# Kernel tuning notes

Hardware: AMD Instinct MI355X
Metric: run time of the kernel (lower is better)

Reference implementation:

```python
import jax, jax.numpy as jnp
import numpy as np
from math import factorial, sqrt

L_MAX = 3
MUL = 64
# e3nn FullyConnectedTensorProduct instruction order: lexicographic over (l1, l2, l3)
# keeping paths with triangle inequality and matching parity ((-1)^(l1+l2) == (-1)^l3).
PATHS = [(l1, l2, l3)
         for l1 in range(L_MAX + 1)
         for l2 in range(L_MAX + 1)
         for l3 in range(L_MAX + 1)
         if abs(l1 - l2) <= l3 <= l1 + l2 and (l1 + l2 + l3) % 2 == 0]
assert len(PATHS) == 23
N_TO = {l3: sum(1 for p in PATHS if p[2] == l3) for l3 in range(L_MAX + 1)}


def _su2_cg(j1, m1, j2, m2, j3, m3):
    # Complex-basis Clebsch-Gordan coefficient (Racah formula), as in e3nn.
    if m3 != m1 + m2:
        return 0.0
    f = factorial
    vmin = max(-j1 + j2 + m3, -j1 + m1, 0)
    vmax = min(j2 + j3 + m1, j3 - j1 + j2, j3 + m3)
    c = sqrt((2 * j3 + 1) * f(j3 + j1 - j2) * f(j3 - j1 + j2) * f(j1 + j2 - j3)
             * f(j3 + m3) * f(j3 - m3)
             / (f(j1 + j2 + j3 + 1) * f(j1 - m1) * f(j1 + m1) * f(j2 - m2) * f(j2 + m2)))
    s = 0.0
    for v in range(vmin, vmax + 1):
        s += (-1) ** (v + j2 + m2) / f(v) * f(j2 + j3 + m1 - v) * f(j1 - m1 + v) \
             / f(j3 - j1 + j2 - v) / f(j3 + m3 - v) / f(v + j1 - j2 - m3)
    return c * s


def _q(l):
    # Change of basis real -> complex spherical harmonics (e3nn convention).
    q = np.zeros((2 * l + 1, 2 * l + 1), dtype=np.complex128)
    for m in range(-l, 0):
        q[l + m, l + abs(m)] = 1.0 / np.sqrt(2.0)
        q[l + m, l - abs(m)] = -1j / np.sqrt(2.0)
    q[l, l] = 1.0
    for m in range(1, l + 1):
        q[l + m, l + abs(m)] = (-1) ** m / np.sqrt(2.0)
        q[l + m, l - abs(m)] = 1j * (-1) ** m / np.sqrt(2.0)
    return (-1j) ** l * q


def _w3j(l1, l2, l3):
    # Real-basis Wigner 3j tensor, unit Frobenius norm (e3nn's o3.wigner_3j).
    csu2 = np.zeros((2 * l1 + 1, 2 * l2 + 1, 2 * l3 + 1))
    for m1 in range(-l1, l1 + 1):
        for m2 in range(-l2, l2 + 1):
            m3 = m1 + m2
            if -l3 <= m3 <= l3:
                csu2[l1 + m1, l2 + m2, l3 + m3] = _su2_cg(l1, m1, l2, m2, l3, m3)
    q1, q2, q3 = _q(l1), _q(l2), _q(l3)
    c = np.einsum('ij,kl,mn,ikn->jlm', q1, q2, np.conj(q3.T), csu2.astype(np.complex128))
    c = np.real(c)
    return (c / np.linalg.norm(c)).astype(np.float32)


W3J = {p: jnp.asarray(_w3j(*p)) for p in PATHS}
# e3nn 'component' irrep_normalization + 'element' path_normalization:
# per-path coeff = sqrt(ir_out.dim / (n_paths_into_out * mul1 * mul2)).
COEFF = {p: float(np.sqrt((2 * p[2] + 1) / (N_TO[p[2]] * MUL * MUL))) for p in PATHS}


def setup_inputs():
    key = jax.random.key(0)
    kx, kw = jax.random.split(key)
    x = jax.random.normal(kx, (2, 1024, MUL * (L_MAX + 1) ** 2), dtype=jnp.float32)
    weights = jax.random.normal(kw, (len(PATHS), MUL, MUL, MUL), dtype=jnp.float32)
    return {"x": x, "weights": weights}


def reference(x, weights):
    B, N, D = x.shape
    Z = B * N
    xf = x.reshape(Z, D)
    # e3nn layout: blocks of (mul, 2l+1) concatenated over l; offset = MUL * l^2.
    xs = [xf[:, MUL * l * l: MUL * (l + 1) ** 2].reshape(Z, MUL, 2 * l + 1)
          for l in range(L_MAX + 1)]
    acc = [jnp.zeros((Z, MUL, 2 * l + 1), dtype=x.dtype) for l in range(L_MAX + 1)]
    for p, (l1, l2, l3) in enumerate(PATHS):
        c = W3J[(l1, l2, l3)]
        t1 = jnp.einsum('zui,ijk->zujk', xs[l1], c)            # [Z,u,2l2+1,2l3+1]
        t2 = jnp.einsum('zujk,zvj->zuvk', t1, xs[l2])          # [Z,u,v,2l3+1]
        seg = jnp.einsum('zuvk,uvw->zwk', t2, weights[p]) * COEFF[(l1, l2, l3)]
        acc[l3] = acc[l3] + seg
    out = jnp.concatenate([a.reshape(Z, -1) for a in acc], axis=-1)
    return out.reshape(B, N, -1)
```

## Files before the change

### kernel.cpp

```cpp
#include <hip/hip_runtime.h>

struct CD { double re, im; };
constexpr CD cmul(CD a, CD b){ return CD{a.re*b.re - a.im*b.im, a.re*b.im + a.im*b.re}; }
constexpr CD conj_(CD a){ return CD{a.re, -a.im}; }

constexpr double factd(int n){ double r = 1.0; for(int i = 2; i <= n; ++i) r *= (double)i; return r; }
constexpr double csqrt_(double x){
  if (x <= 0.0) return 0.0;
  double g = x > 1.0 ? x : 1.0;
  for (int i = 0; i < 100; ++i) g = 0.5*(g + x/g);
  return g;
}

constexpr double su2_cg(int j1,int m1,int j2,int m2,int j3,int m3){
  if (m3 != m1 + m2) return 0.0;
  int vmin = -j1 + j2 + m3;
  if (-j1 + m1 > vmin) vmin = -j1 + m1;
  if (0 > vmin) vmin = 0;
  int vmax = j2 + j3 + m1;
  if (j3 - j1 + j2 < vmax) vmax = j3 - j1 + j2;
  if (j3 + m3 < vmax) vmax = j3 + m3;
  double c = csqrt_((2.0*j3 + 1.0) * factd(j3 + j1 - j2) * factd(j3 - j1 + j2) * factd(j1 + j2 - j3)
                    * factd(j3 + m3) * factd(j3 - m3)
                    / (factd(j1 + j2 + j3 + 1) * factd(j1 - m1) * factd(j1 + m1)
                       * factd(j2 - m2) * factd(j2 + m2)));
  double s = 0.0;
  for (int v = vmin; v <= vmax; ++v){
    double t = (((v + j2 + m2) & 1) ? -1.0 : 1.0) / factd(v)
               * factd(j2 + j3 + m1 - v) * factd(j1 - m1 + v)
               / factd(j3 - j1 + j2 - v) / factd(j3 + m3 - v) / factd(v + j1 - j2 - m3);
    s += t;
  }
  return c * s;
}

struct QM { CD m[7][7]; };
constexpr QM qmat(int l){
  QM q{};
  double is2 = 1.0 / csqrt_(2.0);
  for (int mm = -l; mm < 0; ++mm){
    q.m[l+mm][l-mm] = CD{is2, 0.0};
    q.m[l+mm][l+mm] = CD{0.0, -is2};
  }
  q.m[l][l] = CD{1.0, 0.0};
  for (int mm = 1; mm <= l; ++mm){
    double sgn = (mm & 1) ? -1.0 : 1.0;
    q.m[l+mm][l+mm] = CD{sgn*is2, 0.0};
    q.m[l+mm][l-mm] = CD{0.0, sgn*is2};
  }
  CD ph = (l % 4 == 0) ? CD{1,0} : (l % 4 == 1) ? CD{0,-1} : (l % 4 == 2) ? CD{-1,0} : CD{0,1};
  for (int r = 0; r < 7; ++r)
    for (int c = 0; c < 7; ++c)
      q.m[r][c] = cmul(ph, q.m[r][c]);
  return q;
}

template<int L1,int L2,int L3> struct W3JT { float v[2*L1+1][2*L2+1][2*L3+1]; };

template<int L1,int L2,int L3>
constexpr W3JT<L1,L2,L3> make_w3j(){
  constexpr int D1 = 2*L1+1, D2 = 2*L2+1, D3 = 2*L3+1;
  QM q1 = qmat(L1), q2 = qmat(L2), q3 = qmat(L3);
  double cg[7][7] = {};
  for (int i = 0; i < D1; ++i)
    for (int k = 0; k < D2; ++k){
      int n = i + k - L1 - L2 + L3;
      if (n >= 0 && n < D3) cg[i][k] = su2_cg(L1, i-L1, L2, k-L2, L3, (i-L1)+(k-L2));
    }
  double c[D1][D2][D3] = {};
  double norm2 = 0.0;
  for (int j = 0; j < D1; ++j)
    for (int l = 0; l < D2; ++l)
      for (int m = 0; m < D3; ++m){
        CD s{0.0, 0.0};
        for (int i = 0; i < D1; ++i)
          for (int k = 0; k < D2; ++k){
            double g = cg[i][k];
            if (g == 0.0) continue;
            int n = i + k - L1 - L2 + L3;
            CD t = cmul(q1.m[i][j], q2.m[k][l]);
            t = cmul(t, conj_(q3.m[n][m]));
            s.re += t.re * g; s.im += t.im * g;
          }
        c[j][l][m] = s.re;
        norm2 += s.re * s.re;
      }
  double inv = 1.0 / csqrt_(norm2);
  W3JT<L1,L2,L3> w{};
  for (int j = 0; j < D1; ++j)
    for (int l = 0; l < D2; ++l)
      for (int m = 0; m < D3; ++m){
        double val = c[j][l][m] * inv;
        if (val < 1e-10 && val > -1e-10) val = 0.0;
        w.v[j][l][m] = (float)val;
      }
  return w;
}

__device__ __constant__ int L3P_[23]  = {0,1,2,3,1,0,2,1,3,2,2,1,3,0,2,1,3,3,2,1,3,0,2};
__device__ __constant__ int SWAPP_[23] = {0,1,1,1,0,0,0,1,1,1,0,0,0,0,0,1,1,0,0,0,0,0,0};
constexpr int K3CUM[24] = {0,1,4,9,16,19,20,25,28,35,40,45,48,55,56,61,64,71,78,83,86,93,94,99};
constexpr size_t KSLICE = 2048ull * 64ull;

typedef __bf16 bf16x8 __attribute__((ext_vector_type(8)));
typedef float  f32x4  __attribute__((ext_vector_type(4)));
typedef float  f32x2  __attribute__((ext_vector_type(2)));

__global__ void pack_w_kernel(const float* __restrict__ w, unsigned short* __restrict__ wp, int total){
  int idx = blockIdx.x * 256 + threadIdx.x;
  if (idx >= total) return;
  int e    = idx & 7;
  int lane = (idx >> 3) & 63;
  int nt   = (idx >> 9) & 3;
  int hf   = (idx >> 11) & 1;
  int s    = (idx >> 12) & 63;
  int p    = idx >> 18;
  int kv = hf*32 + (lane >> 4)*8 + e;
  int wc = nt*16 + (lane & 15);
  int l3 = L3P_[p];
  const float nto[4] = {4.f, 6.f, 7.f, 6.f};
  float coeff = sqrtf((2.f*l3 + 1.f) / (nto[l3] * 4096.f));
  int a = SWAPP_[p] ? kv : s;
  int b = SWAPP_[p] ? s : kv;
  float val = w[(((size_t)p*64 + a)*64 + b)*64 + wc] * coeff;
  unsigned bits = __builtin_bit_cast(unsigned, val);
  unsigned r = (bits + 0x7FFFu + ((bits >> 16) & 1u)) >> 16;
  wp[idx] = (unsigned short)r;
}

__global__ void transpose_x(const float* __restrict__ x, float* __restrict__ xT){
  __shared__ float t[32][33];
  int bx = blockIdx.x, by = blockIdx.y;
  int tx = threadIdx.x & 31, ty = threadIdx.x >> 5;
  #pragma unroll
  for (int r = 0; r < 4; ++r)
    t[ty + r*8][tx] = x[(size_t)(by*32 + ty + r*8)*1024 + bx*32 + tx];
  __syncthreads();
  #pragma unroll
  for (int r = 0; r < 4; ++r)
    xT[(size_t)(bx*32 + ty + r*8)*2048 + by*32 + tx] = t[tx][ty + r*8];
}

template<int P,int L1,int L2,int L3,bool SWAP,int G0,int G,bool PART>
__device__ __forceinline__ void run_slot(
    int tile, const float* __restrict__ xT,
    const unsigned short* __restrict__ wp,
    float* __restrict__ dst, float* red)
{
  constexpr int K3 = 2*L3+1;
  constexpr int LK = SWAP ? L1 : L2;
  constexpr int LS = SWAP ? L2 : L1;
  constexpr int DK = 2*LK+1, DS = 2*LS+1;
  constexpr auto C = make_w3j<L1,L2,L3>();

  const int lane = threadIdx.x & 63;
  const int wv   = threadIdx.x >> 6;
  const int zc   = tile*16 + (lane & 15);

  f32x2 xk2[4][DK];
  {
    const float* xkb = xT + (size_t)(64*LK*LK)*2048 + zc;
    const int t0 = wv*32 + (lane >> 4)*8;
    #pragma unroll
    for (int q = 0; q < 4; ++q)
      #pragma unroll
      for (int t = 0; t < DK; ++t){
        float lo = xkb[(size_t)((t0 + 2*q    )*DK + t)*2048];
        float hi = xkb[(size_t)((t0 + 2*q + 1)*DK + t)*2048];
        xk2[q][t] = f32x2{lo, hi};
      }
  }

  const float* xsb = xT + (size_t)(64*LS*LS)*2048 + zc;
  const unsigned short* wu = wp + (size_t)P*262144 + (size_t)wv*2048 + (size_t)lane*8;

  f32x4 acc[G][4];
  #pragma unroll
  for (int a = 0; a < G; ++a)
    #pragma unroll
    for (int b = 0; b < 4; ++b) acc[a][b] = f32x4{0.f,0.f,0.f,0.f};

  auto compute = [&](const bf16x8 (&bf)[4], const float (&xs)[DS]){
    #pragma unroll
    for (int kk = 0; kk < G; ++kk){
      float dk[DK];
      #pragma unroll
      for (int t = 0; t < DK; ++t) dk[t] = 0.f;
      #pragma unroll
      for (int t = 0; t < DK; ++t){
        #pragma unroll
        for (int j = 0; j < DS; ++j){
          const float cv = SWAP ? C.v[t][j][G0+kk] : C.v[j][t][G0+kk];
          if (cv != 0.0f) dk[t] = __builtin_fmaf(xs[j], cv, dk[t]);
        }
      }
      f32x2 af2[4];
      #pragma unroll
      for (int q = 0; q < 4; ++q) af2[q] = f32x2{0.f, 0.f};
      #pragma unroll
      for (int t = 0; t < DK; ++t){
        const f32x2 d2 = f32x2{dk[t], dk[t]};
        #pragma unroll
        for (int q = 0; q < 4; ++q)
          af2[q] += xk2[q][t] * d2;
      }
      bf16x8 af;
      #pragma unroll
      for (int q = 0; q < 4; ++q){
        af[2*q]   = (__bf16)af2[q].x;
        af[2*q+1] = (__bf16)af2[q].y;
      }
      __builtin_amdgcn_s_setprio(1);
      #pragma unroll
      for (int nt = 0; nt < 4; ++nt)
        acc[kk][nt] = __builtin_amdgcn_mfma_f32_16x16x32_bf16(af, bf[nt], acc[kk][nt], 0, 0, 0);
      __builtin_amdgcn_s_setprio(0);
    }
  };

  bf16x8 bA[4], bB[4];
  float xsA[DS], xsB[DS];
  #pragma unroll
  for (int nt = 0; nt < 4; ++nt)
    bA[nt] = *reinterpret_cast<const bf16x8*>(wu + nt*512);
  #pragma unroll
  for (int j = 0; j < DS; ++j) xsA[j] = xsb[(size_t)j*2048];

  for (int s = 0; s < 64; s += 2){
    #pragma unroll
    for (int nt = 0; nt < 4; ++nt)
      bB[nt] = *reinterpret_cast<const bf16x8*>(wu + 4096 + nt*512);
    #pragma unroll
    for (int j = 0; j < DS; ++j) xsB[j] = xsb[(size_t)(DS + j)*2048];

    compute(bA, xsA);

    #pragma unroll
    for (int nt = 0; nt < 4; ++nt)
      bA[nt] = *reinterpret_cast<const bf16x8*>(wu + 8192 + nt*512);
    #pragma unroll
    for (int j = 0; j < DS; ++j) xsA[j] = xsb[(size_t)(2*DS + j)*2048];

    compute(bB, xsB);

    wu  += 8192;
    xsb += (size_t)2*DS*2048;
  }

  constexpr int Gh = (G + 1) / 2;
  static_assert(Gh <= 3, "red[] sized for Gh<=3");
  auto store_one = [&](int kk, int nt, const f32x4& o, const f32x4& a){
    #pragma unroll
    for (int r = 0; r < 4; ++r){
      int zl = ((lane >> 4) << 2) + r;
      int wc = nt*16 + (lane & 15);
      float val = a[r] + o[r];
      if constexpr (PART){
        dst[(size_t)(K3CUM[P] + G0 + kk)*KSLICE + (size_t)(tile*16 + zl)*64 + wc] = val;
      } else {
        unsafeAtomicAdd(dst + (size_t)(tile*16 + zl)*1024 + 64*L3*L3 + wc*K3 + (G0+kk), val);
      }
    }
  };

  if (wv == 1){
    #pragma unroll
    for (int kk = 0; kk < Gh; ++kk)
      #pragma unroll
      for (int nt = 0; nt < 4; ++nt)
        *reinterpret_cast<f32x4*>(&red[((kk*4 + nt)*64 + lane)*4]) = acc[kk][nt];
  }
  __syncthreads();
  if (wv == 0){
    #pragma unroll
    for (int kk = 0; kk < Gh; ++kk)
      #pragma unroll
      for (int nt = 0; nt < 4; ++nt){
        f32x4 o = *reinterpret_cast<const f32x4*>(&red[((kk*4 + nt)*64 + lane)*4]);
        store_one(kk, nt, o, acc[kk][nt]);
      }
  }
  if constexpr (G > Gh){
    if (wv == 0){
      #pragma unroll
      for (int kk = Gh; kk < G; ++kk)
        #pragma unroll
        for (int nt = 0; nt < 4; ++nt)
          *reinterpret_cast<f32x4*>(&red[(((kk-Gh)*4 + nt)*64 + lane)*4]) = acc[kk][nt];
    }
    __syncthreads();
    if (wv == 1){
      #pragma unroll
      for (int kk = Gh; kk < G; ++kk)
        #pragma unroll
        for (int nt = 0; nt < 4; ++nt){
          f32x4 o = *reinterpret_cast<const f32x4*>(&red[(((kk-Gh)*4 + nt)*64 + lane)*4]);
          store_one(kk, nt, o, acc[kk][nt]);
        }
    }
  }
}

template<bool PART>
__global__ __launch_bounds__(128, 3) void tp_main(const float* __restrict__ xT,
    const unsigned short* __restrict__ wp, float* __restrict__ dst)
{
  __shared__ __align__(16) float red[3072];
  const int slot = blockIdx.x >> 7;
  const int tile = blockIdx.x & 127;
  switch (slot){
    case 0:  run_slot< 6,1,1,2,false,0,5,PART>(tile,xT,wp,dst,red); break;
    case 1:  run_slot<16,2,3,3,true ,0,3,PART>(tile,xT,wp,dst,red); break;
    case 2:  run_slot<20,3,2,3,false,0,3,PART>(tile,xT,wp,dst,red); break;
    case 3:  run_slot<14,2,2,2,false,0,3,PART>(tile,xT,wp,dst,red); break;
    case 4:  run_slot<15,2,3,1,true ,0,3,PART>(tile,xT,wp,dst,red); break;
    case 5:  run_slot<19,3,2,1,false,0,3,PART>(tile,xT,wp,dst,red); break;
    case 6:  run_slot< 8,1,2,3,true ,0,4,PART>(tile,xT,wp,dst,red); break;
    case 7:  run_slot<12,2,1,3,false,0,4,PART>(tile,xT,wp,dst,red); break;
    case 8:  run_slot<22,3,3,2,false,0,2,PART>(tile,xT,wp,dst,red); break;
    case 9:  run_slot<22,3,3,2,false,2,2,PART>(tile,xT,wp,dst,red); break;
    case 10: run_slot< 9,1,3,2,true ,0,3,PART>(tile,xT,wp,dst,red); break;
    case 11: run_slot<16,2,3,3,true ,3,2,PART>(tile,xT,wp,dst,red); break;
    case 12: run_slot<16,2,3,3,true ,5,2,PART>(tile,xT,wp,dst,red); break;
    case 13: run_slot<20,3,2,3,false,3,2,PART>(tile,xT,wp,dst,red); break;
    case 14: run_slot<20,3,2,3,false,5,2,PART>(tile,xT,wp,dst,red); break;
    case 15: run_slot< 2,0,2,2,true ,0,5,PART>(tile,xT,wp,dst,red); break;
    case 16: run_slot<10,2,0,2,false,0,5,PART>(tile,xT,wp,dst,red); break;
    case 17: run_slot<11,2,1,1,false,0,3,PART>(tile,xT,wp,dst,red); break;
    case 18: run_slot< 7,1,2,1,true ,0,3,PART>(tile,xT,wp,dst,red); break;
    case 19: run_slot<18,3,1,2,false,0,3,PART>(tile,xT,wp,dst,red); break;
    case 20: run_slot< 8,1,2,3,true ,4,3,PART>(tile,xT,wp,dst,red); break;
    case 21: run_slot<12,2,1,3,false,4,3,PART>(tile,xT,wp,dst,red); break;
    case 22: run_slot<14,2,2,2,false,3,2,PART>(tile,xT,wp,dst,red); break;
    case 23: run_slot< 9,1,3,2,true ,3,2,PART>(tile,xT,wp,dst,red); break;
    case 24: run_slot<18,3,1,2,false,3,2,PART>(tile,xT,wp,dst,red); break;
    case 25: run_slot<22,3,3,2,false,4,1,PART>(tile,xT,wp,dst,red); break;
    case 26: run_slot<21,3,3,0,false,0,1,PART>(tile,xT,wp,dst,red); break;
    case 27: run_slot< 3,0,3,3,true ,0,4,PART>(tile,xT,wp,dst,red); break;
    case 28: run_slot<17,3,0,3,false,0,4,PART>(tile,xT,wp,dst,red); break;
    case 29: run_slot< 3,0,3,3,true ,4,3,PART>(tile,xT,wp,dst,red); break;
    case 30: run_slot<17,3,0,3,false,4,3,PART>(tile,xT,wp,dst,red); break;
    case 31: run_slot< 1,0,1,1,true ,0,3,PART>(tile,xT,wp,dst,red); break;
    case 32: run_slot< 4,1,0,1,false,0,3,PART>(tile,xT,wp,dst,red); break;
    case 33: run_slot<13,2,2,0,false,0,1,PART>(tile,xT,wp,dst,red); break;
    case 34: run_slot< 5,1,1,0,false,0,1,PART>(tile,xT,wp,dst,red); break;
    case 35: run_slot< 0,0,0,0,false,0,1,PART>(tile,xT,wp,dst,red); break;
    default: break;
  }
}

__global__ void gather_out(const float* __restrict__ part, float* __restrict__ out){
  const int z = blockIdx.x;
  const int t = threadIdx.x;
  const int w = t & 63;
  const int g = t >> 6;
  const size_t zw = (size_t)z*64 + w;
  const float* pb = part;
  auto rd = [&](int kg){ return pb[(size_t)kg*KSLICE + zw]; };
  float* ob = out + (size_t)z*1024;
  if (g == 0){
    ob[w] = rd(K3CUM[0]) + rd(K3CUM[5]) + rd(K3CUM[13]) + rd(K3CUM[21]);
  } else if (g == 1){
    #pragma unroll
    for (int k = 0; k < 3; ++k)
      ob[64 + w*3 + k] = rd(K3CUM[1]+k) + rd(K3CUM[4]+k) + rd(K3CUM[7]+k)
                       + rd(K3CUM[11]+k) + rd(K3CUM[15]+k) + rd(K3CUM[19]+k);
  } else if (g == 2){
    #pragma unroll
    for (int k = 0; k < 5; ++k)
      ob[256 + w*5 + k] = rd(K3CUM[2]+k) + rd(K3CUM[6]+k) + rd(K3CUM[9]+k)
                        + rd(K3CUM[10]+k) + rd(K3CUM[14]+k) + rd(K3CUM[18]+k)
                        + rd(K3CUM[22]+k);
  } else {
    #pragma unroll
    for (int k = 0; k < 7; ++k)
      ob[576 + w*7 + k] = rd(K3CUM[3]+k) + rd(K3CUM[8]+k) + rd(K3CUM[12]+k)
                        + rd(K3CUM[16]+k) + rd(K3CUM[17]+k) + rd(K3CUM[20]+k);
  }
}

extern "C" void kernel_launch(void* const* d_in, const int* in_sizes, int n_in,
                              void* d_out, int out_size, void* d_ws, size_t ws_size,
                              hipStream_t stream)
{
  const float* x = (const float*)d_in[0];
  const float* w = (const float*)d_in[1];
  float* out = (float*)d_out;

  const size_t packB = 23ull*64*2*4*64*8 * sizeof(unsigned short);
  const size_t xTB   = 1024ull*2048*sizeof(float);
  const size_t partB = 99ull*KSLICE*sizeof(float);
  const size_t slack = 65536;
  const int totalW = 23*64*2*4*64*8;

  unsigned short* wp = (unsigned short*)d_ws;
  float* xT   = (float*)((char*)d_ws + packB);
  float* part = (float*)((char*)d_ws + packB + xTB);

  if (ws_size < packB + xTB + slack) return;

  pack_w_kernel<<<(totalW + 255)/256, 256, 0, stream>>>(w, wp, totalW);
  dim3 tg(32, 64);
  transpose_x<<<tg, 256, 0, stream>>>(x, xT);

  if (ws_size >= packB + xTB + partB + slack){
    tp_main<true><<<36*128, 128, 0, stream>>>(xT, wp, part);
    gather_out<<<2048, 256, 0, stream>>>(part, out);
  } else {
    hipMemsetAsync(d_out, 0, (size_t)out_size * sizeof(float), stream);
    tp_main<false><<<36*128, 128, 0, stream>>>(xT, wp, out);
  }
}
```

Baseline: 222.7 us.

## Split work so each wave owns a full K range for two z-tiles

Most blocks now use a run_full path in which each of the two waves handles its own 16-row z tile and covers both K halves of the weight, which removes the cross-wave LDS reduction and one barrier. The m3 components are regrouped into many more slots, mostly G=1 or 2. Only the 3-3-x paths keep the half-K split with a sequential reduction. The partial buffer layout changes to (z, k, w) ordering, staged through LDS for coalesced stores, and the double-buffered prefetch loop is replaced by a single-step prefetch. In exchange, weight fragments are reloaded more times in total and register pressure rises from holding both K-half x fragments.

After: 228.5 us. 2.6% more time.

```diff
diff --git a/kernel.cpp b/kernel.cpp
--- a/kernel.cpp
+++ b/kernel.cpp
@@ -100,7 +100,7 @@
 __device__ __constant__ int L3P_[23]  = {0,1,2,3,1,0,2,1,3,2,2,1,3,0,2,1,3,3,2,1,3,0,2};
 __device__ __constant__ int SWAPP_[23] = {0,1,1,1,0,0,0,1,1,1,0,0,0,0,0,1,1,0,0,0,0,0,0};
 constexpr int K3CUM[24] = {0,1,4,9,16,19,20,25,28,35,40,45,48,55,56,61,64,71,78,83,86,93,94,99};
-constexpr size_t KSLICE = 2048ull * 64ull;
+constexpr size_t PSLICE = 2048ull * 64ull;
 
 typedef __bf16 bf16x8 __attribute__((ext_vector_type(8)));
 typedef float  f32x4  __attribute__((ext_vector_type(4)));
@@ -142,7 +142,139 @@
 }
 
 template<int P,int L1,int L2,int L3,bool SWAP,int G0,int G,bool PART>
-__device__ __forceinline__ void run_slot(
+__device__ __forceinline__ void run_full(
+    int tile2, const float* __restrict__ xT,
+    const unsigned short* __restrict__ wp,
+    float* __restrict__ dst, float* lds)
+{
+  constexpr int K3 = 2*L3+1;
+  constexpr int LK = SWAP ? L1 : L2;
+  constexpr int LS = SWAP ? L2 : L1;
+  constexpr int DK = 2*LK+1, DS = 2*LS+1;
+  constexpr auto C = make_w3j<L1,L2,L3>();
+
+  const int lane = threadIdx.x & 63;
+  const int wid  = threadIdx.x >> 6;
+  const int z0   = (tile2*2 + wid)*16;
+  const int zc   = z0 + (lane & 15);
+
+  f32x2 xkl[4][DK], xkh[4][DK];
+  {
+    const float* xkb = xT + (size_t)(64*LK*LK)*2048 + zc;
+    const int t0 = (lane >> 4)*8;
+    #pragma unroll
+    for (int q = 0; q < 4; ++q)
+      #pragma unroll
+      for (int t = 0; t < DK; ++t){
+        xkl[q][t] = f32x2{ xkb[(size_t)((t0 + 2*q    )*DK + t)*2048],
+                           xkb[(size_t)((t0 + 2*q + 1)*DK + t)*2048] };
+        xkh[q][t] = f32x2{ xkb[(size_t)((32 + t0 + 2*q    )*DK + t)*2048],
+                           xkb[(size_t)((32 + t0 + 2*q + 1)*DK + t)*2048] };
+      }
+  }
+
+  const float* xsp = xT + (size_t)(64*LS*LS)*2048 + zc;
+  const unsigned short* wu = wp + (size_t)P*262144 + (size_t)lane*8;
+
+  f32x4 acc[G][4];
+  #pragma unroll
+  for (int a = 0; a < G; ++a)
+    #pragma unroll
+    for (int b = 0; b < 4; ++b) acc[a][b] = f32x4{0.f,0.f,0.f,0.f};
+
+  float xs[DS];
+  #pragma unroll
+  for (int j = 0; j < DS; ++j) xs[j] = xsp[(size_t)j*2048];
+
+  for (int s = 0; s < 64; ++s){
+    bf16x8 bl[4], bh[4];
+    #pragma unroll
+    for (int nt = 0; nt < 4; ++nt){
+      bl[nt] = *reinterpret_cast<const bf16x8*>(wu + nt*512);
+      bh[nt] = *reinterpret_cast<const bf16x8*>(wu + 2048 + nt*512);
+    }
+    const float* xnp = (s < 63) ? xsp + (size_t)DS*2048 : xsp;
+    float xn[DS];
+    #pragma unroll
+    for (int j = 0; j < DS; ++j) xn[j] = xnp[(size_t)j*2048];
+
+    #pragma unroll
+    for (int kk = 0; kk < G; ++kk){
+      float dk[DK];
+      #pragma unroll
+      for (int t = 0; t < DK; ++t) dk[t] = 0.f;
+      #pragma unroll
+      for (int t = 0; t < DK; ++t){
+        #pragma unroll
+        for (int j = 0; j < DS; ++j){
+          const float cv = SWAP ? C.v[t][j][G0+kk] : C.v[j][t][G0+kk];
+          if (cv != 0.0f) dk[t] = __builtin_fmaf(xs[j], cv, dk[t]);
+        }
+      }
+      f32x2 al2[4], ah2[4];
+      #pragma unroll
+      for (int q = 0; q < 4; ++q){ al2[q] = f32x2{0.f,0.f}; ah2[q] = f32x2{0.f,0.f}; }
+      #pragma unroll
+      for (int t = 0; t < DK; ++t){
+        const f32x2 d2 = f32x2{dk[t], dk[t]};
+        #pragma unroll
+        for (int q = 0; q < 4; ++q){
+          al2[q] += xkl[q][t] * d2;
+          ah2[q] += xkh[q][t] * d2;
+        }
+      }
+      bf16x8 afl, afh;
+      #pragma unroll
+      for (int q = 0; q < 4; ++q){
+        afl[2*q] = (__bf16)al2[q].x;  afl[2*q+1] = (__bf16)al2[q].y;
+        afh[2*q] = (__bf16)ah2[q].x;  afh[2*q+1] = (__bf16)ah2[q].y;
+      }
+      __builtin_amdgcn_s_setprio(1);
+      #pragma unroll
+      for (int nt = 0; nt < 4; ++nt){
+        acc[kk][nt] = __builtin_amdgcn_mfma_f32_16x16x32_bf16(afl, bl[nt], acc[kk][nt], 0, 0, 0);
+        acc[kk][nt] = __builtin_amdgcn_mfma_f32_16x16x32_bf16(afh, bh[nt], acc[kk][nt], 0, 0, 0);
+      }
+      __builtin_amdgcn_s_setprio(0);
+    }
+    #pragma unroll
+    for (int j = 0; j < DS; ++j) xs[j] = xn[j];
+    xsp += (size_t)DS*2048;
+    wu  += 4096;
+  }
+
+  if constexpr (PART){
+    float* tl = lds + wid*1040;
+    #pragma unroll
+    for (int kk = 0; kk < G; ++kk){
+      #pragma unroll
+      for (int nt = 0; nt < 4; ++nt)
+        #pragma unroll
+        for (int r = 0; r < 4; ++r)
+          tl[((lane>>4)*4 + r)*65 + nt*16 + (lane & 15)] = acc[kk][nt][r];
+      #pragma unroll
+      for (int zr = 0; zr < 16; ++zr){
+        float v = tl[zr*65 + lane];
+        dst[(size_t)K3CUM[P]*PSLICE + ((size_t)(z0 + zr)*K3 + (G0+kk))*64 + lane] = v;
+      }
+    }
+  } else {
+    #pragma unroll
+    for (int kk = 0; kk < G; ++kk)
+      #pragma unroll
+      for (int nt = 0; nt < 4; ++nt)
+        #pragma unroll
+        for (int r = 0; r < 4; ++r){
+          int zl = (lane>>4)*4 + r;
+          int wc = nt*16 + (lane & 15);
+          unsafeAtomicAdd(dst + (size_t)(z0 + zl)*1024 + 64*L3*L3 + wc*K3 + (G0+kk),
+                          acc[kk][nt][r]);
+        }
+  }
+}
+
+template<int P,int L1,int L2,int L3,bool SWAP,int G0,int G,bool PART>
+__device__ __forceinline__ void run_half(
     int tile, const float* __restrict__ xT,
     const unsigned short* __restrict__ wp,
     float* __restrict__ dst, float* red)
@@ -152,6 +284,7 @@
   constexpr int LS = SWAP ? L2 : L1;
   constexpr int DK = 2*LK+1, DS = 2*LS+1;
   constexpr auto C = make_w3j<L1,L2,L3>();
+  static_assert(G <= 2, "run_half sized for G<=2");
 
   const int lane = threadIdx.x & 63;
   const int wv   = threadIdx.x >> 6;
@@ -164,14 +297,12 @@
     #pragma unroll
     for (int q = 0; q < 4; ++q)
       #pragma unroll
-      for (int t = 0; t < DK; ++t){
-        float lo = xkb[(size_t)((t0 + 2*q    )*DK + t)*2048];
-        float hi = xkb[(size_t)((t0 + 2*q + 1)*DK + t)*2048];
-        xk2[q][t] = f32x2{lo, hi};
-      }
-  }
-
-  const float* xsb = xT + (size_t)(64*LS*LS)*2048 + zc;
+      for (int t = 0; t < DK; ++t)
+        xk2[q][t] = f32x2{ xkb[(size_t)((t0 + 2*q    )*DK + t)*2048],
+                           xkb[(size_t)((t0 + 2*q + 1)*DK + t)*2048] };
+  }
+
+  const float* xsp = xT + (size_t)(64*LS*LS)*2048 + zc;
   const unsigned short* wu = wp + (size_t)P*262144 + (size_t)wv*2048 + (size_t)lane*8;
 
   f32x4 acc[G][4];
@@ -180,7 +311,21 @@
     #pragma unroll
     for (int b = 0; b < 4; ++b) acc[a][b] = f32x4{0.f,0.f,0.f,0.f};
 
-  auto compute = [&](const bf16x8 (&bf)[4], const float (&xs)[DS]){
+  float xs[DS];
+  #pragma unroll
+  for (int j = 0; j < DS; ++j) xs[j] = xsp[(size_t)j*2048];
+
+  for (int s = 0; s < 64; ++s){
+    bf16x8 bfrag[4];
+    #pragma unroll
+    for (int nt = 0; nt < 4; ++nt)
+      bfrag[nt] = *reinterpret_cast<const bf16x8*>(wu + nt*512);
+
+    const float* xnp = (s < 63) ? xsp + (size_t)DS*2048 : xsp;
+    float xn[DS];
+    #pragma unroll
+    for (int j = 0; j < DS; ++j) xn[j] = xnp[(size_t)j*2048];
+
     #pragma unroll
     for (int kk = 0; kk < G; ++kk){
       float dk[DK];
@@ -213,42 +358,15 @@
       __builtin_amdgcn_s_setprio(1);
       #pragma unroll
       for (int nt = 0; nt < 4; ++nt)
-        acc[kk][nt] = __builtin_amdgcn_mfma_f32_16x16x32_bf16(af, bf[nt], acc[kk][nt], 0, 0, 0);
+        acc[kk][nt] = __builtin_amdgcn_mfma_f32_16x16x32_bf16(af, bfrag[nt], acc[kk][nt], 0, 0, 0);
       __builtin_amdgcn_s_setprio(0);
     }
-  };
-
-  bf16x8 bA[4], bB[4];
-  float xsA[DS], xsB[DS];
-  #pragma unroll
-  for (int nt = 0; nt < 4; ++nt)
-    bA[nt] = *reinterpret_cast<const bf16x8*>(wu + nt*512);
-  #pragma unroll
-  for (int j = 0; j < DS; ++j) xsA[j] = xsb[(size_t)j*2048];
-
-  for (int s = 0; s < 64; s += 2){
-    #pragma unroll
-    for (int nt = 0; nt < 4; ++nt)
-      bB[nt] = *reinterpret_cast<const bf16x8*>(wu + 4096 + nt*512);
-    #pragma unroll
-    for (int j = 0; j < DS; ++j) xsB[j] = xsb[(size_t)(DS + j)*2048];
-
-    compute(bA, xsA);
-
-    #pragma unroll
-    for (int nt = 0; nt < 4; ++nt)
-      bA[nt] = *reinterpret_cast<const bf16x8*>(wu + 8192 + nt*512);
-    #pragma unroll
-    for (int j = 0; j < DS; ++j) xsA[j] = xsb[(size_t)(2*DS + j)*2048];
-
-    compute(bB, xsB);
-
-    wu  += 8192;
-    xsb += (size_t)2*DS*2048;
-  }
-
-  constexpr int Gh = (G + 1) / 2;
-  static_assert(Gh <= 3, "red[] sized for Gh<=3");
+    #pragma unroll
+    for (int j = 0; j < DS; ++j) xs[j] = xn[j];
+    xsp += (size_t)DS*2048;
+    wu  += 4096;
+  }
+
   auto store_one = [&](int kk, int nt, const f32x4& o, const f32x4& a){
     #pragma unroll
     for (int r = 0; r < 4; ++r){
@@ -256,7 +374,7 @@
       int wc = nt*16 + (lane & 15);
       float val = a[r] + o[r];
       if constexpr (PART){
-        dst[(size_t)(K3CUM[P] + G0 + kk)*KSLICE + (size_t)(tile*16 + zl)*64 + wc] = val;
+        dst[(size_t)K3CUM[P]*PSLICE + ((size_t)(tile*16 + zl)*K3 + (G0+kk))*64 + wc] = val;
       } else {
         unsafeAtomicAdd(dst + (size_t)(tile*16 + zl)*1024 + 64*L3*L3 + wc*K3 + (G0+kk), val);
       }
@@ -265,38 +383,31 @@
 
   if (wv == 1){
     #pragma unroll
-    for (int kk = 0; kk < Gh; ++kk)
-      #pragma unroll
-      for (int nt = 0; nt < 4; ++nt)
-        *reinterpret_cast<f32x4*>(&red[((kk*4 + nt)*64 + lane)*4]) = acc[kk][nt];
+    for (int nt = 0; nt < 4; ++nt)
+      *reinterpret_cast<f32x4*>(&red[(nt*64 + lane)*4]) = acc[0][nt];
   }
   __syncthreads();
   if (wv == 0){
     #pragma unroll
-    for (int kk = 0; kk < Gh; ++kk)
-      #pragma unroll
-      for (int nt = 0; nt < 4; ++nt){
-        f32x4 o = *reinterpret_cast<const f32x4*>(&red[((kk*4 + nt)*64 + lane)*4]);
-        store_one(kk, nt, o, acc[kk][nt]);
-      }
-  }
-  if constexpr (G > Gh){
+    for (int nt = 0; nt < 4; ++nt){
+      f32x4 o = *reinterpret_cast<const f32x4*>(&red[(nt*64 + lane)*4]);
+      store_one(0, nt, o, acc[0][nt]);
+    }
+  }
+  if constexpr (G > 1){
+    __syncthreads();
     if (wv == 0){
       #pragma unroll
-      for (int kk = Gh; kk < G; ++kk)
-        #pragma unroll
-        for (int nt = 0; nt < 4; ++nt)
-          *reinterpret_cast<f32x4*>(&red[(((kk-Gh)*4 + nt)*64 + lane)*4]) = acc[kk][nt];
+      for (int nt = 0; nt < 4; ++nt)
+        *reinterpret_cast<f32x4*>(&red[(nt*64 + lane)*4]) = acc[1][nt];
     }
     __syncthreads();
     if (wv == 1){
       #pragma unroll
-      for (int kk = Gh; kk < G; ++kk)
-        #pragma unroll
-        for (int nt = 0; nt < 4; ++nt){
-          f32x4 o = *reinterpret_cast<const f32x4*>(&red[(((kk-Gh)*4 + nt)*64 + lane)*4]);
-          store_one(kk, nt, o, acc[kk][nt]);
-        }
+      for (int nt = 0; nt < 4; ++nt){
+        f32x4 o = *reinterpret_cast<const f32x4*>(&red[(nt*64 + lane)*4]);
+        store_one(1, nt, o, acc[1][nt]);
+      }
     }
   }
 }
@@ -305,46 +416,82 @@
 __global__ __launch_bounds__(128, 3) void tp_main(const float* __restrict__ xT,
     const unsigned short* __restrict__ wp, float* __restrict__ dst)
 {
-  __shared__ __align__(16) float red[3072];
-  const int slot = blockIdx.x >> 7;
-  const int tile = blockIdx.x & 127;
+  __shared__ __align__(16) float lds[2080];
+  if (blockIdx.x < 512){
+    const int fslot = blockIdx.x >> 7;
+    const int tile  = blockIdx.x & 127;
+    switch (fslot){
+      case 0: run_half<22,3,3,2,false,0,2,PART>(tile,xT,wp,dst,lds); break;
+      case 1: run_half<22,3,3,2,false,2,2,PART>(tile,xT,wp,dst,lds); break;
+      case 2: run_half<22,3,3,2,false,4,1,PART>(tile,xT,wp,dst,lds); break;
+      case 3: run_half<21,3,3,0,false,0,1,PART>(tile,xT,wp,dst,lds); break;
+      default: break;
+    }
+    return;
+  }
+  const int idx   = blockIdx.x - 512;
+  const int slot  = idx >> 6;
+  const int tile2 = idx & 63;
   switch (slot){
-    case 0:  run_slot< 6,1,1,2,false,0,5,PART>(tile,xT,wp,dst,red); break;
-    case 1:  run_slot<16,2,3,3,true ,0,3,PART>(tile,xT,wp,dst,red); break;
-    case 2:  run_slot<20,3,2,3,false,0,3,PART>(tile,xT,wp,dst,red); break;
-    case 3:  run_slot<14,2,2,2,false,0,3,PART>(tile,xT,wp,dst,red); break;
-    case 4:  run_slot<15,2,3,1,true ,0,3,PART>(tile,xT,wp,dst,red); break;
-    case 5:  run_slot<19,3,2,1,false,0,3,PART>(tile,xT,wp,dst,red); break;
-    case 6:  run_slot< 8,1,2,3,true ,0,4,PART>(tile,xT,wp,dst,red); break;
-    case 7:  run_slot<12,2,1,3,false,0,4,PART>(tile,xT,wp,dst,red); break;
-    case 8:  run_slot<22,3,3,2,false,0,2,PART>(tile,xT,wp,dst,red); break;
-    case 9:  run_slot<22,3,3,2,false,2,2,PART>(tile,xT,wp,dst,red); break;
-    case 10: run_slot< 9,1,3,2,true ,0,3,PART>(tile,xT,wp,dst,red); break;
-    case 11: run_slot<16,2,3,3,true ,3,2,PART>(tile,xT,wp,dst,red); break;
-    case 12: run_slot<16,2,3,3,true ,5,2,PART>(tile,xT,wp,dst,red); break;
-    case 13: run_slot<20,3,2,3,false,3,2,PART>(tile,xT,wp,dst,red); break;
-    case 14: run_slot<20,3,2,3,false,5,2,PART>(tile,xT,wp,dst,red); break;
-    case 15: run_slot< 2,0,2,2,true ,0,5,PART>(tile,xT,wp,dst,red); break;
-    case 16: run_slot<10,2,0,2,false,0,5,PART>(tile,xT,wp,dst,red); break;
-    case 17: run_slot<11,2,1,1,false,0,3,PART>(tile,xT,wp,dst,red); break;
-    case 18: run_slot< 7,1,2,1,true ,0,3,PART>(tile,xT,wp,dst,red); break;
-    case 19: run_slot<18,3,1,2,false,0,3,PART>(tile,xT,wp,dst,red); break;
-    case 20: run_slot< 8,1,2,3,true ,4,3,PART>(tile,xT,wp,dst,red); break;
-    case 21: run_slot<12,2,1,3,false,4,3,PART>(tile,xT,wp,dst,red); break;
-    case 22: run_slot<14,2,2,2,false,3,2,PART>(tile,xT,wp,dst,red); break;
-    case 23: run_slot< 9,1,3,2,true ,3,2,PART>(tile,xT,wp,dst,red); break;
-    case 24: run_slot<18,3,1,2,false,3,2,PART>(tile,xT,wp,dst,red); break;
-    case 25: run_slot<22,3,3,2,false,4,1,PART>(tile,xT,wp,dst,red); break;
-    case 26: run_slot<21,3,3,0,false,0,1,PART>(tile,xT,wp,dst,red); break;
-    case 27: run_slot< 3,0,3,3,true ,0,4,PART>(tile,xT,wp,dst,red); break;
-    case 28: run_slot<17,3,0,3,false,0,4,PART>(tile,xT,wp,dst,red); break;
-    case 29: run_slot< 3,0,3,3,true ,4,3,PART>(tile,xT,wp,dst,red); break;
-    case 30: run_slot<17,3,0,3,false,4,3,PART>(tile,xT,wp,dst,red); break;
-    case 31: run_slot< 1,0,1,1,true ,0,3,PART>(tile,xT,wp,dst,red); break;
-    case 32: run_slot< 4,1,0,1,false,0,3,PART>(tile,xT,wp,dst,red); break;
-    case 33: run_slot<13,2,2,0,false,0,1,PART>(tile,xT,wp,dst,red); break;
-    case 34: run_slot< 5,1,1,0,false,0,1,PART>(tile,xT,wp,dst,red); break;
-    case 35: run_slot< 0,0,0,0,false,0,1,PART>(tile,xT,wp,dst,red); break;
+    case 0:  run_full<16,2,3,3,true ,0,1,PART>(tile2,xT,wp,dst,lds); break;
+    case 1:  run_full<16,2,3,3,true ,1,1,PART>(tile2,xT,wp,dst,lds); break;
+    case 2:  run_full<16,2,3,3,true ,2,1,PART>(tile2,xT,wp,dst,lds); break;
+    case 3:  run_full<16,2,3,3,true ,3,1,PART>(tile2,xT,wp,dst,lds); break;
+    case 4:  run_full<16,2,3,3,true ,4,1,PART>(tile2,xT,wp,dst,lds); break;
+    case 5:  run_full<16,2,3,3,true ,5,1,PART>(tile2,xT,wp,dst,lds); break;
+    case 6:  run_full<16,2,3,3,true ,6,1,PART>(tile2,xT,wp,dst,lds); break;
+    case 7:  run_full<20,3,2,3,false,0,1,PART>(tile2,xT,wp,dst,lds); break;
+    case 8:  run_full<20,3,2,3,false,1,1,PART>(tile2,xT,wp,dst,lds); break;
+    case 9:  run_full<20,3,2,3,false,2,1,PART>(tile2,xT,wp,dst,lds); break;
+    case 10: run_full<20,3,2,3,false,3,1,PART>(tile2,xT,wp,dst,lds); break;
+    case 11: run_full<20,3,2,3,false,4,1,PART>(tile2,xT,wp,dst,lds); break;
+    case 12: run_full<20,3,2,3,false,5,1,PART>(tile2,xT,wp,dst,lds); break;
+    case 13: run_full<20,3,2,3,false,6,1,PART>(tile2,xT,wp,dst,lds); break;
+    case 14: run_full<15,2,3,1,true ,0,1,PART>(tile2,xT,wp,dst,lds); break;
+    case 15: run_full<15,2,3,1,true ,1,1,PART>(tile2,xT,wp,dst,lds); break;
+    case 16: run_full<15,2,3,1,true ,2,1,PART>(tile2,xT,wp,dst,lds); break;
+    case 17: run_full<19,3,2,1,false,0,1,PART>(tile2,xT,wp,dst,lds); break;
+    case 18: run_full<19,3,2,1,false,1,1,PART>(tile2,xT,wp,dst,lds); break;
+    case 19: run_full<19,3,2,1,false,2,1,PART>(tile2,xT,wp,dst,lds); break;
+    case 20: run_full<14,2,2,2,false,0,1,PART>(tile2,xT,wp,dst,lds); break;
+    case 21: run_full<14,2,2,2,false,1,1,PART>(tile2,xT,wp,dst,lds); break;
+    case 22: run_full<14,2,2,2,false,2,1,PART>(tile2,xT,wp,dst,lds); break;
+    case 23: run_full<14,2,2,2,false,3,1,PART>(tile2,xT,wp,dst,lds); break;
+    case 24: run_full<14,2,2,2,false,4,1,PART>(tile2,xT,wp,dst,lds); break;
+    case 25: run_full<13,2,2,0,false,0,1,PART>(tile2,xT,wp,dst,lds); break;
+    case 26: run_full< 8,1,2,3,true ,0,2,PART>(tile2,xT,wp,dst,lds); break;
+    case 27: run_full< 8,1,2,3,true ,2,2,PART>(tile2,xT,wp,dst,lds); break;
+    case 28: run_full< 8,1,2,3,true ,4,2,PART>(tile2,xT,wp,dst,lds); break;
+    case 29: run_full< 8,1,2,3,true ,6,1,PART>(tile2,xT,wp,dst,lds); break;
+    case 30: run_full<12,2,1,3,false,0,2,PART>(tile2,xT,wp,dst,lds); break;
+    case 31: run_full<12,2,1,3,false,2,2,PART>(tile2,xT,wp,dst,lds); break;
+    case 32: run_full<12,2,1,3,false,4,2,PART>(tile2,xT,wp,dst,lds); break;
+    case 33: run_full<12,2,1,3,false,6,1,PART>(tile2,xT,wp,dst,lds); break;
+    case 34: run_full< 6,1,1,2,false,0,2,PART>(tile2,xT,wp,dst,lds); break;
+    case 35: run_full< 6,1,1,2,false,2,2,PART>(tile2,xT,wp,dst,lds); break;
+    case 36: run_full< 6,1,1,2,false,4,1,PART>(tile2,xT,wp,dst,lds); break;
+    case 37: run_full< 9,1,3,2,true ,0,2,PART>(tile2,xT,wp,dst,lds); break;
+    case 38: run_full< 9,1,3,2,true ,2,2,PART>(tile2,xT,wp,dst,lds); break;
+    case 39: run_full< 9,1,3,2,true ,4,1,PART>(tile2,xT,wp,dst,lds); break;
+    case 40: run_full<18,3,1,2,false,0,2,PART>(tile2,xT,wp,dst,lds); break;
+    case 41: run_full<18,3,1,2,false,2,2,PART>(tile2,xT,wp,dst,lds); break;
+    case 42: run_full<18,3,1,2,false,4,1,PART>(tile2,xT,wp,dst,lds); break;
+    case 43: run_full< 7,1,2,1,true ,0,2,PART>(tile2,xT,wp,dst,lds); break;
+    case 44: run_full< 7,1,2,1,true ,2,1,PART>(tile2,xT,wp,dst,lds); break;
+    case 45: run_full<11,2,1,1,false,0,2,PART>(tile2,xT,wp,dst,lds); break;
+    case 46: run_full<11,2,1,1,false,2,1,PART>(tile2,xT,wp,dst,lds); break;
+    case 47: run_full< 5,1,1,0,false,0,1,PART>(tile2,xT,wp,dst,lds); break;
+    case 48: run_full< 3,0,3,3,true ,0,4,PART>(tile2,xT,wp,dst,lds); break;
+    case 49: run_full< 3,0,3,3,true ,4,3,PART>(tile2,xT,wp,dst,lds); break;
+    case 50: run_full<17,3,0,3,false,0,4,PART>(tile2,xT,wp,dst,lds); break;
+    case 51: run_full<17,3,0,3,false,4,3,PART>(tile2,xT,wp,dst,lds); break;
+    case 52: run_full< 2,0,2,2,true ,0,3,PART>(tile2,xT,wp,dst,lds); break;
+    case 53: run_full< 2,0,2,2,true ,3,2,PART>(tile2,xT,wp,dst,lds); break;
+    case 54: run_full<10,2,0,2,false,0,3,PART>(tile2,xT,wp,dst,lds); break;
+    case 55: run_full<10,2,0,2,false,3,2,PART>(tile2,xT,wp,dst,lds); break;
+    case 56: run_full< 1,0,1,1,true ,0,3,PART>(tile2,xT,wp,dst,lds); break;
+    case 57: run_full< 4,1,0,1,false,0,3,PART>(tile2,xT,wp,dst,lds); break;
+    case 58: run_full< 0,0,0,0,false,0,1,PART>(tile2,xT,wp,dst,lds); break;
     default: break;
   }
 }
@@ -354,28 +501,27 @@
   const int t = threadIdx.x;
   const int w = t & 63;
   const int g = t >> 6;
-  const size_t zw = (size_t)z*64 + w;
-  const float* pb = part;
-  auto rd = [&](int kg){ return pb[(size_t)kg*KSLICE + zw]; };
   float* ob = out + (size_t)z*1024;
+  auto rd = [&](int p, int K3p, int k){
+    return part[(size_t)K3CUM[p]*PSLICE + ((size_t)z*K3p + k)*64 + w];
+  };
   if (g == 0){
-    ob[w] = rd(K3CUM[0]) + rd(K3CUM[5]) + rd(K3CUM[13]) + rd(K3CUM[21]);
+    ob[w] = rd(0,1,0) + rd(5,1,0) + rd(13,1,0) + rd(21,1,0);
   } else if (g == 1){
     #pragma unroll
     for (int k = 0; k < 3; ++k)
-      ob[64 + w*3 + k] = rd(K3CUM[1]+k) + rd(K3CUM[4]+k) + rd(K3CUM[7]+k)
-                       + rd(K3CUM[11]+k) + rd(K3CUM[15]+k) + rd(K3CUM[19]+k);
+      ob[64 + w*3 + k] = rd(1,3,k) + rd(4,3,k) + rd(7,3,k)
+                       + rd(11,3,k) + rd(15,3,k) + rd(19,3,k);
   } else if (g == 2){
     #pragma unroll
     for (int k = 0; k < 5; ++k)
-      ob[256 + w*5 + k] = rd(K3CUM[2]+k) + rd(K3CUM[6]+k) + rd(K3CUM[9]+k)
-                        + rd(K3CUM[10]+k) + rd(K3CUM[14]+k) + rd(K3CUM[18]+k)
-                        + rd(K3CUM[22]+k);
+      ob[256 + w*5 + k] = rd(2,5,k) + rd(6,5,k) + rd(9,5,k) + rd(10,5,k)
+                        + rd(14,5,k) + rd(18,5,k) + rd(22,5,k);
   } else {
     #pragma unroll
     for (int k = 0; k < 7; ++k)
-      ob[576 + w*7 + k] = rd(K3CUM[3]+k) + rd(K3CUM[8]+k) + rd(K3CUM[12]+k)
-                        + rd(K3CUM[16]+k) + rd(K3CUM[17]+k) + rd(K3CUM[20]+k);
+      ob[576 + w*7 + k] = rd(3,7,k) + rd(8,7,k) + rd(12,7,k)
+                        + rd(16,7,k) + rd(17,7,k) + rd(20,7,k);
   }
 }
 
@@ -389,25 +535,25 @@
 
   const size_t packB = 23ull*64*2*4*64*8 * sizeof(unsigned short);
   const size_t xTB   = 1024ull*2048*sizeof(float);
-  const size_t partB = 99ull*KSLICE*sizeof(float);
-  const size_t slack = 65536;
+  const size_t partB = 99ull*PSLICE*sizeof(float);
   const int totalW = 23*64*2*4*64*8;
 
   unsigned short* wp = (unsigned short*)d_ws;
   float* xT   = (float*)((char*)d_ws + packB);
   float* part = (float*)((char*)d_ws + packB + xTB);
 
-  if (ws_size < packB + xTB + slack) return;
+  if (ws_size < packB + xTB) return;
 
   pack_w_kernel<<<(totalW + 255)/256, 256, 0, stream>>>(w, wp, totalW);
   dim3 tg(32, 64);
   transpose_x<<<tg, 256, 0, stream>>>(x, xT);
 
-  if (ws_size >= packB + xTB + partB + slack){
-    tp_main<true><<<36*128, 128, 0, stream>>>(xT, wp, part);
+  const int nblocks = 512 + 59*64;
+  if (ws_size >= packB + xTB + partB){
+    tp_main<true><<<nblocks, 128, 0, stream>>>(xT, wp, part);
     gather_out<<<2048, 256, 0, stream>>>(part, out);
   } else {
     hipMemsetAsync(d_out, 0, (size_t)out_size * sizeof(float), stream);
-    tp_main<false><<<36*128, 128, 0, stream>>>(xT, wp, out);
-  }
-}
+    tp_main<false><<<nblocks, 128, 0, stream>>>(xT, wp, out);
+  }
+}
```
